# Optimization experiments

Measured on AMD Instinct MI355X. Metric: run time of the kernel, lower is better.

## Reference

```python
import jax, jax.numpy as jnp
import numpy as np

N_HEAD = 16

def setup_inputs() -> dict:
    key = jax.random.key(0)
    k1, k2, k3 = jax.random.split(key, 3)
    B, T, C = 4, 2048, 1024
    x = jax.random.normal(k1, (B, T, C), dtype=jnp.float32)
    W_qkv = jax.random.normal(k2, (3 * C, C), dtype=jnp.float32) * 0.02
    W_o = jax.random.normal(k3, (C, C), dtype=jnp.float32) * (0.02 / np.sqrt(2.0))
    return {"x": x, "W_qkv": W_qkv, "W_o": W_o}

def reference(x, W_qkv, W_o):
    B, T, C = x.shape
    H = N_HEAD
    d_k = C // H
    # combined qkv projection (torch Linear: y = x @ W^T)
    qkv = x @ W_qkv.T                      # (B, T, 3C)
    q, k, v = jnp.split(qkv, 3, axis=-1)
    def split_heads(t):
        return t.reshape(B, T, H, d_k).transpose(0, 2, 1, 3)  # (B, H, T, d_k)
    q, k, v = split_heads(q), split_heads(k), split_heads(v)
    scale = 1.0 / jnp.sqrt(jnp.asarray(d_k, dtype=x.dtype))
    scores = jnp.einsum('bhqd,bhkd->bhqk', q, k) * scale      # (B, H, T, T)
    causal = jnp.tril(jnp.ones((T, T), dtype=bool))           # True = keep
    scores = jnp.where(causal[None, None], scores, -jnp.inf)
    attn = jax.nn.softmax(scores, axis=-1)                    # no NaNs under causal mask
    out = jnp.einsum('bhqk,bhkd->bhqd', attn, v)              # (B, H, T, d_k)
    out = out.transpose(0, 2, 1, 3).reshape(B, T, C)
    return out @ W_o.T
```

## Files before the change

kernel.cpp:

```cpp
#include <hip/hip_runtime.h>
#include <hip/hip_bf16.h>
#include <cstdint>

typedef __bf16 bf16;
typedef __bf16 bf16x8 __attribute__((ext_vector_type(8)));
typedef float f32x4 __attribute__((ext_vector_type(4)));

#define MFMA16(A, B, C) __builtin_amdgcn_mfma_f32_16x16x32_bf16((A), (B), (C), 0, 0, 0)

__device__ __forceinline__ void async16(const bf16* g, bf16* l) {
    __builtin_amdgcn_global_load_lds(
        (const __attribute__((address_space(1))) void*)g,
        (__attribute__((address_space(3))) void*)l, 16, 0, 0);
}

__global__ void cvt_all(const float* __restrict__ x, const float* __restrict__ wq,
                        const float* __restrict__ wo, bf16* __restrict__ xb,
                        bf16* __restrict__ wqb, bf16* __restrict__ wob) {
    const int bid = blockIdx.x;
    const float* s;
    bf16* d;
    int off;
    if (bid < 4096)      { s = x;  d = xb;  off = bid; }
    else if (bid < 5632) { s = wq; d = wqb; off = bid - 4096; }
    else                 { s = wo; d = wob; off = bid - 5632; }
    const size_t i = ((size_t)off * 256 + threadIdx.x) * 8;
    const float4 a = *(const float4*)(s + i);
    const float4 b2 = *(const float4*)(s + i + 4);
    bf16x8 r;
    r[0] = (bf16)a.x; r[1] = (bf16)a.y; r[2] = (bf16)a.z; r[3] = (bf16)a.w;
    r[4] = (bf16)b2.x; r[5] = (bf16)b2.y; r[6] = (bf16)b2.z; r[7] = (bf16)b2.w;
    *(bf16x8*)(d + i) = r;
}

template <int MODE>
__launch_bounds__(256, 3)
__global__ void gemm_nt(const bf16* __restrict__ A, const bf16* __restrict__ Bm,
                        void* __restrict__ O0, bf16* __restrict__ O1,
                        bf16* __restrict__ O2, int N, int K) {
    __shared__ alignas(16) bf16 SM[2][128 * 64];
    bf16* const As = SM[0];
    bf16* const Bs = SM[1];

    const int t = threadIdx.x;
    const int w = t >> 6, l = t & 63, quad = l >> 4, l15 = l & 15;
    const int wm = w & 1, wn = w >> 1;

    const int gx = (int)gridDim.x;
    const int nwg = gx * (int)gridDim.y;
    const int wg0 = (int)blockIdx.y * gx + (int)blockIdx.x;
    const int wg = (wg0 & 7) * (nwg >> 3) + (wg0 >> 3);
    const int m0 = (wg / gx) * 128, n0 = (wg % gx) * 128;

    f32x4 acc[4][4] = {};

    const int srow = t >> 3, sch = t & 7;
    const bf16* ga = A + (size_t)(m0 + srow) * K + sch * 8;
    const bf16* gb = Bm + (size_t)(n0 + srow) * K + sch * 8;

    for (int kt = 0; kt < K; kt += 64) {
        __syncthreads();
#pragma unroll
        for (int i = 0; i < 4; i++) {
            async16(ga + (size_t)i * 32 * K + kt, &As[(i * 256 + t) * 8]);
            async16(gb + (size_t)i * 32 * K + kt, &Bs[(i * 256 + t) * 8]);
        }
        __syncthreads();

#pragma unroll
        for (int s = 0; s < 2; s++) {
            bf16x8 af[4], bfr[4];
#pragma unroll
            for (int im = 0; im < 4; im++)
                af[im] = *(const bf16x8*)&As[(wm * 64 + im * 16 + l15) * 64 + s * 32 + quad * 8];
#pragma unroll
            for (int in = 0; in < 4; in++)
                bfr[in] = *(const bf16x8*)&Bs[(wn * 64 + in * 16 + l15) * 64 + s * 32 + quad * 8];
#pragma unroll
            for (int im = 0; im < 4; im++)
#pragma unroll
                for (int in = 0; in < 4; in++)
                    acc[im][in] = MFMA16(af[im], bfr[in], acc[im][in]);
        }
    }

    if (MODE == 0) {
        if (n0 >= 2048) {
            __syncthreads();
            bf16* const Ts = &SM[0][0];
#pragma unroll
            for (int in = 0; in < 4; in++) {
                const int col = wn * 64 + in * 16 + l15;
                const int cx = (col & 7) << 3;
#pragma unroll
                for (int im = 0; im < 4; im++) {
                    const int row0 = (wm * 64 + im * 16 + quad * 4) ^ cx;
#pragma unroll
                    for (int r = 0; r < 4; r++)
                        Ts[col * 128 + row0 + r] = (bf16)acc[im][in][r];
                }
            }
            __syncthreads();
            bf16* VtOut = O2;
            const int bb = m0 >> 11, tt0 = m0 & 2047;
            const int c0 = n0 - 2048;
#pragma unroll
            for (int p = 0; p < 8; p++) {
                const int col = p * 16 + w * 4 + (l >> 4);
                const int chunk = l & 15;
                const int physc = ((chunk ^ (col & 7)) & 7) + (chunk & 8);
                const bf16x8 v = *(const bf16x8*)&Ts[col * 128 + physc * 8];
                const int cg = c0 + col, h = cg >> 6, d = cg & 63;
                *(bf16x8*)&VtOut[((size_t)(bb * 16 + h) * 64 + d) * 2048 + tt0 + chunk * 8] = v;
            }
        } else {
            bf16* Q0 = (bf16*)O0;
#pragma unroll
            for (int in = 0; in < 4; in++) {
                const int n = n0 + wn * 64 + in * 16;
                const int sel = n >> 10;
                const int c = n & 1023;
                const int h = c >> 6;
                const int dd = c & 63;
                bf16* dst = (sel == 0) ? Q0 : O1;
#pragma unroll
                for (int im = 0; im < 4; im++) {
#pragma unroll
                    for (int r = 0; r < 4; r++) {
                        const int m = m0 + wm * 64 + im * 16 + quad * 4 + r;
                        const int b = m >> 11, tt = m & 2047;
                        dst[((size_t)(b * 16 + h) * 2048 + tt) * 64 + dd + l15] =
                            (bf16)acc[im][in][r];
                    }
                }
            }
        }
    } else {
        float* Of = (float*)O0;
#pragma unroll
        for (int im = 0; im < 4; im++) {
#pragma unroll
            for (int in = 0; in < 4; in++) {
#pragma unroll
                for (int r = 0; r < 4; r++) {
                    const int m = m0 + wm * 64 + im * 16 + quad * 4 + r;
                    const int n = n0 + wn * 64 + in * 16 + l15;
                    Of[(size_t)m * N + n] = acc[im][in][r];
                }
            }
        }
    }
}

__launch_bounds__(256, 4)
__global__ void attn_fwd(const bf16* __restrict__ Q, const bf16* __restrict__ Kk,
                         const bf16* __restrict__ Vt, bf16* __restrict__ O) {
    __shared__ alignas(16) bf16 Ks[64 * 72];
    __shared__ alignas(16) bf16 Vs[64 * 72];

    const int t = threadIdx.x, w = t >> 6, l = t & 63;
    const int quad = l >> 4, l15 = l & 15;
    const int bh = blockIdx.x, pair = blockIdx.y;
    const int b = bh >> 4, h = bh & 15;
    const int sr = t >> 3, sc = t & 7;

    const bf16* Qbase = Q + (size_t)bh * 2048 * 64;
    const bf16* Kbase = Kk + (size_t)bh * 2048 * 64;
    const bf16* Vbase = Vt + (size_t)bh * 64 * 2048;

    const int qt0 = pair, qt1 = 31 - pair;

    int kr[4];
#pragma unroll
    for (int nt = 0; nt < 4; nt++)
        kr[nt] = (nt >> 1) * 32 + (l15 >> 2) * 8 + (nt & 1) * 4 + (l15 & 3);

    bf16x8 aq[2][2];
#pragma unroll
    for (int hf = 0; hf < 2; hf++) {
        const int qrow = (hf ? qt1 : qt0) * 64 + w * 16 + l15;
        aq[hf][0] = *(const bf16x8*)&Qbase[(size_t)qrow * 64 + quad * 8];
        aq[hf][1] = *(const bf16x8*)&Qbase[(size_t)qrow * 64 + 32 + quad * 8];
#pragma unroll
        for (int j = 0; j < 8; j++) {
            aq[hf][0][j] = aq[hf][0][j] * (bf16)0.1803369f;
            aq[hf][1][j] = aq[hf][1][j] * (bf16)0.1803369f;
        }
    }

    bf16x8 ones;
#pragma unroll
    for (int j = 0; j < 8; j++) ones[j] = (bf16)1.0f;

    f32x4 liacc[2] = {};
    f32x4 oa[2][4] = {};

    bf16x8 rk0 = *(const bf16x8*)&Kbase[(size_t)sr * 64 + sc * 8];
    bf16x8 rk1 = *(const bf16x8*)&Kbase[(size_t)(sr + 32) * 64 + sc * 8];
    bf16x8 rv0 = *(const bf16x8*)&Vbase[(size_t)sr * 2048 + sc * 8];
    bf16x8 rv1 = *(const bf16x8*)&Vbase[(size_t)(sr + 32) * 2048 + sc * 8];

    for (int kt = 0; kt <= qt1; kt++) {
        __syncthreads();
        *(bf16x8*)&Ks[sr * 72 + sc * 8] = rk0;
        *(bf16x8*)&Ks[(sr + 32) * 72 + sc * 8] = rk1;
        *(bf16x8*)&Vs[sr * 72 + sc * 8] = rv0;
        *(bf16x8*)&Vs[(sr + 32) * 72 + sc * 8] = rv1;
        __syncthreads();

        if (kt < qt1) {
            const int kn = kt + 1;
            rk0 = *(const bf16x8*)&Kbase[(size_t)(kn * 64 + sr) * 64 + sc * 8];
            rk1 = *(const bf16x8*)&Kbase[(size_t)(kn * 64 + sr + 32) * 64 + sc * 8];
            rv0 = *(const bf16x8*)&Vbase[(size_t)sr * 2048 + kn * 64 + sc * 8];
            rv1 = *(const bf16x8*)&Vbase[(size_t)(sr + 32) * 2048 + kn * 64 + sc * 8];
        }

        const bool do0 = (kt <= qt0);

        bf16x8 ap[2][2];
#pragma unroll
        for (int np = 0; np < 2; np++) {
            bf16x8 ka[2][2];
#pragma unroll
            for (int i = 0; i < 2; i++) {
                ka[i][0] = *(const bf16x8*)&Ks[kr[2 * np + i] * 72 + quad * 8];
                ka[i][1] = *(const bf16x8*)&Ks[kr[2 * np + i] * 72 + 32 + quad * 8];
            }
#pragma unroll
            for (int hf = 0; hf < 2; hf++) {
                if (hf == 0 && !do0) continue;
                const bool diag = (kt == (hf ? qt1 : qt0));
#pragma unroll
                for (int i = 0; i < 2; i++) {
                    f32x4 s = {};
                    s = MFMA16(ka[i][0], aq[hf][0], s);
                    s = MFMA16(ka[i][1], aq[hf][1], s);
                    const int kbase = np * 32 + quad * 8 + i * 4;
#pragma unroll
                    for (int r = 0; r < 4; r++) {
                        float x = s[r];
                        if (diag && (kbase + r) > (w * 16 + l15)) x = -1e30f;
                        ap[hf][np][i * 4 + r] = (bf16)__builtin_amdgcn_exp2f(x);
                    }
                }
            }
        }

#pragma unroll
        for (int s2 = 0; s2 < 2; s2++) {
            if (do0) liacc[0] = MFMA16(ap[0][s2], ones, liacc[0]);
            liacc[1] = MFMA16(ap[1][s2], ones, liacc[1]);
#pragma unroll
            for (int dt = 0; dt < 4; dt++) {
                bf16x8 bv = *(const bf16x8*)&Vs[(dt * 16 + l15) * 72 + s2 * 32 + quad * 8];
                if (do0) oa[0][dt] = MFMA16(ap[0][s2], bv, oa[0][dt]);
                oa[1][dt] = MFMA16(ap[1][s2], bv, oa[1][dt]);
            }
        }
    }

#pragma unroll
    for (int hf = 0; hf < 2; hf++) {
        const int qt = hf ? qt1 : qt0;
#pragma unroll
        for (int r = 0; r < 4; r++) {
            const float inv = __builtin_amdgcn_rcpf(liacc[hf][r]);
            const int m = b * 2048 + qt * 64 + w * 16 + quad * 4 + r;
#pragma unroll
            for (int dt = 0; dt < 4; dt++) {
                O[(size_t)m * 1024 + h * 64 + dt * 16 + l15] = (bf16)(oa[hf][dt][r] * inv);
            }
        }
    }
}

extern "C" void kernel_launch(void* const* d_in, const int* in_sizes, int n_in,
                              void* d_out, int out_size, void* d_ws, size_t ws_size,
                              hipStream_t stream) {
    const float* x = (const float*)d_in[0];
    const float* wqkv = (const float*)d_in[1];
    const float* wo = (const float*)d_in[2];

    const size_t SZ = (size_t)8192 * 1024;
    bf16* xb = (bf16*)d_ws;
    bf16* wqb = xb + SZ;
    bf16* wob = wqb + (size_t)3072 * 1024;
    bf16* Qw = wob + (size_t)1024 * 1024;
    bf16* Kw = Qw + SZ;
    bf16* Vtw = Kw + SZ;

    dim3 blk(256);
    cvt_all<<<6144, blk, 0, stream>>>(x, wqkv, wo, xb, wqb, wob);
    gemm_nt<0><<<dim3(24, 64), blk, 0, stream>>>(xb, wqb, Qw, Kw, Vtw, 3072, 1024);
    attn_fwd<<<dim3(64, 16), blk, 0, stream>>>(Qw, Kw, Vtw, xb);
    gemm_nt<1><<<dim3(8, 64), blk, 0, stream>>>(xb, wob, d_out, nullptr, nullptr, 1024, 1024);
}
```

Baseline: 227.5 us.

## Read K and V tiles directly from global memory in attention loop

Removes the shared-memory staging of K and V tiles, along with the register prefetch and the two block barriers per key tile. Each wave now loads its MFMA operands straight from global memory and relies on the cache to serve the repeats across the four waves. This trades barrier and LDS traffic for redundant global/L2 loads that are not prefetched, so load latency is exposed inside the loop.

```diff
diff --git a/kernel.cpp b/kernel.cpp
--- a/kernel.cpp
+++ b/kernel.cpp
@@ -155,14 +155,10 @@
 __launch_bounds__(256, 4)
 __global__ void attn_fwd(const bf16* __restrict__ Q, const bf16* __restrict__ Kk,
                          const bf16* __restrict__ Vt, bf16* __restrict__ O) {
-    __shared__ alignas(16) bf16 Ks[64 * 72];
-    __shared__ alignas(16) bf16 Vs[64 * 72];
-
     const int t = threadIdx.x, w = t >> 6, l = t & 63;
     const int quad = l >> 4, l15 = l & 15;
     const int bh = blockIdx.x, pair = blockIdx.y;
     const int b = bh >> 4, h = bh & 15;
-    const int sr = t >> 3, sc = t & 7;
 
     const bf16* Qbase = Q + (size_t)bh * 2048 * 64;
     const bf16* Kbase = Kk + (size_t)bh * 2048 * 64;
@@ -195,27 +191,9 @@
     f32x4 liacc[2] = {};
     f32x4 oa[2][4] = {};
 
-    bf16x8 rk0 = *(const bf16x8*)&Kbase[(size_t)sr * 64 + sc * 8];
-    bf16x8 rk1 = *(const bf16x8*)&Kbase[(size_t)(sr + 32) * 64 + sc * 8];
-    bf16x8 rv0 = *(const bf16x8*)&Vbase[(size_t)sr * 2048 + sc * 8];
-    bf16x8 rv1 = *(const bf16x8*)&Vbase[(size_t)(sr + 32) * 2048 + sc * 8];
-
     for (int kt = 0; kt <= qt1; kt++) {
-        __syncthreads();
-        *(bf16x8*)&Ks[sr * 72 + sc * 8] = rk0;
-        *(bf16x8*)&Ks[(sr + 32) * 72 + sc * 8] = rk1;
-        *(bf16x8*)&Vs[sr * 72 + sc * 8] = rv0;
-        *(bf16x8*)&Vs[(sr + 32) * 72 + sc * 8] = rv1;
-        __syncthreads();
-
-        if (kt < qt1) {
-            const int kn = kt + 1;
-            rk0 = *(const bf16x8*)&Kbase[(size_t)(kn * 64 + sr) * 64 + sc * 8];
-            rk1 = *(const bf16x8*)&Kbase[(size_t)(kn * 64 + sr + 32) * 64 + sc * 8];
-            rv0 = *(const bf16x8*)&Vbase[(size_t)sr * 2048 + kn * 64 + sc * 8];
-            rv1 = *(const bf16x8*)&Vbase[(size_t)(sr + 32) * 2048 + kn * 64 + sc * 8];
-        }
-
+        const bf16* Kt = Kbase + (size_t)kt * 64 * 64;
+        const bf16* Vc = Vbase + (size_t)kt * 64;
         const bool do0 = (kt <= qt0);
 
         bf16x8 ap[2][2];
@@ -224,8 +202,9 @@
             bf16x8 ka[2][2];
 #pragma unroll
             for (int i = 0; i < 2; i++) {
-                ka[i][0] = *(const bf16x8*)&Ks[kr[2 * np + i] * 72 + quad * 8];
-                ka[i][1] = *(const bf16x8*)&Ks[kr[2 * np + i] * 72 + 32 + quad * 8];
+                const int row = kr[2 * np + i];
+                ka[i][0] = *(const bf16x8*)&Kt[row * 64 + quad * 8];
+                ka[i][1] = *(const bf16x8*)&Kt[row * 64 + 32 + quad * 8];
             }
 #pragma unroll
             for (int hf = 0; hf < 2; hf++) {
@@ -253,7 +232,8 @@
             liacc[1] = MFMA16(ap[1][s2], ones, liacc[1]);
 #pragma unroll
             for (int dt = 0; dt < 4; dt++) {
-                bf16x8 bv = *(const bf16x8*)&Vs[(dt * 16 + l15) * 72 + s2 * 32 + quad * 8];
+                bf16x8 bv = *(const bf16x8*)&Vc[(size_t)(dt * 16 + l15) * 2048 +
+                                                s2 * 32 + quad * 8];
                 if (do0) oa[0][dt] = MFMA16(ap[0][s2], bv, oa[0][dt]);
                 oa[1][dt] = MFMA16(ap[1][s2], bv, oa[1][dt]);
             }
```

Measured after the change: 367.3 us. +61.5%, slower.
